# Kernel tuning notes

Hardware: AMD Instinct MI355X
Metric: run time of the kernel (lower is better)

Reference implementation:

```python
import jax, jax.numpy as jnp
import numpy as np

B, N, D = 512, 120, 64
NB = 8  # n_freq_bands
S_CLIP, DELTA_CLIP = 10.0, 5.0


def zc_rms(x, g, eps=1e-8):
    # zero-centred RMS norm
    x0 = x - x0_mean(x)
    return x0 * jax.lax.rsqrt(jnp.mean(x0 * x0, axis=-1, keepdims=True) + eps) * g


def x0_mean(x):
    return jnp.mean(x, axis=-1, keepdims=True)


def l2norm(x, eps=1e-8):
    return x * jax.lax.rsqrt(jnp.sum(x * x, axis=-1, keepdims=True) + eps)


def setup_inputs() -> dict:
    key = jax.random.key(0)
    ks = jax.random.split(key, 12)
    s = 1.0 / np.sqrt(D)
    return {
        "x": jax.random.normal(ks[0], (B, N, D), dtype=jnp.float32),
        "g_norm": jnp.ones((D,), jnp.float32),
        "Wq": jax.random.normal(ks[1], (D, D), jnp.float32) * s,
        "Wk": jax.random.normal(ks[2], (D, D), jnp.float32) * s,
        "Wv": jax.random.normal(ks[3], (D, D), jnp.float32) * s,
        "bv": jnp.zeros((D,), jnp.float32),
        "Wo": jax.random.normal(ks[4], (D, D), jnp.float32) * s,
        "bo": jnp.zeros((D,), jnp.float32),
        "g_post": jnp.ones((D,), jnp.float32),
        "W1": jax.random.normal(ks[5], (NB, 16), jnp.float32) * (1.0 / np.sqrt(NB)),
        "b1": jnp.zeros((16,), jnp.float32),
        "W2": jax.random.normal(ks[6], (16, 1), jnp.float32) * 0.25,
        "b2": jnp.full((1,), 0.5, jnp.float32),  # bias init 0.5 as in torch
    }


def _gamma(h, W1, b1, W2, b2):
    # FFT over embedding dim, band-averaged energies -> gate in [0.5, 0.99]
    fft = jnp.abs(jnp.fft.rfft(jax.lax.stop_gradient(h), axis=-1))  # (B,N,n_f)
    n_f = fft.shape[-1]
    bs = max(1, n_f // NB)
    bands = [fft[..., i * bs:min(i * bs + bs, n_f)].mean(-1) for i in range(NB)]
    energy = jnp.stack(bands, axis=-1)  # (B,N,NB)
    energy = energy / jnp.clip(jnp.sum(energy, axis=-1, keepdims=True), 1e-8)
    hdn = jax.nn.silu(energy @ W1 + b1)
    raw = jax.nn.sigmoid(hdn @ W2 + b2)  # (B,N,1)
    return 0.5 + 0.49 * raw


def reference(x, g_norm, Wq, Wk, Wv, bv, Wo, bo, g_post, W1, b1, W2, b2):
    h = zc_rms(x, g_norm)
    q = l2norm(h @ Wq)
    k = l2norm(h @ Wk)
    v = h @ Wv + bv
    gamma = _gamma(h, W1, b1, W2, b2)  # (B,N,1)

    # time-major for scan
    qT = jnp.moveaxis(q, 1, 0)      # (N,B,D)
    kT = jnp.moveaxis(k, 1, 0)
    vT = jnp.moveaxis(v, 1, 0)
    gT = jnp.moveaxis(gamma, 1, 0)  # (N,B,1)

    S0 = jnp.zeros((x.shape[0], D, D), x.dtype)

    def step(S, inp):
        q_t, k_t, v_t, g_t = inp
        pred = jnp.einsum('bde,be->bd', S, k_t)
        delta = jnp.clip(v_t - pred, -DELTA_CLIP, DELTA_CLIP)
        S = g_t[..., None] * S + delta[:, :, None] * k_t[:, None, :]
        S = jnp.clip(S, -S_CLIP, S_CLIP)
        o_t = jnp.einsum('bde,be->bd', S, q_t)
        return S, o_t

    _, outT = jax.lax.scan(step, S0, (qT, kT, vT, gT))
    out = jnp.moveaxis(outT, 0, 1)  # (B,N,D)
    out = zc_rms(out, g_post) @ Wo + bo  # dropout is identity at inference
    return x + out
```

## Files before the change

### kernel.cpp

```cpp
#include <hip/hip_runtime.h>
#include <math.h>

#define B_ 512
#define N_ 120

typedef __attribute__((ext_vector_type(8))) _Float16 f16x8;
typedef __attribute__((ext_vector_type(2))) _Float16 f16x2;
typedef __attribute__((ext_vector_type(4))) float f32x4;

#define OFF_WQ 0
#define OFF_WK 4096
#define OFF_WV 8192
#define OFF_T  12288
#define OFF_XF 16384
#define OFF_QS 0
#define OFF_KS 7680
#define OFF_VS 15360
#define OFF_OF 23040
#define OFF_WO 31232
#define LDS_F16 35328

__device__ __forceinline__ void mm4(f16x8 a0, f16x8 a1, const _Float16* wmat,
                                    int lane, f32x4* acc) {
    const f16x8* wv = (const f16x8*)wmat;
    #pragma unroll
    for (int nt = 0; nt < 4; ++nt) {
        f32x4 z = {0.f, 0.f, 0.f, 0.f};
        z = __builtin_amdgcn_mfma_f32_16x16x32_f16(a0, wv[nt * 128 + lane], z, 0, 0, 0);
        z = __builtin_amdgcn_mfma_f32_16x16x32_f16(a1, wv[nt * 128 + 64 + lane], z, 0, 0, 0);
        acc[nt] = z;
    }
}

__global__ __launch_bounds__(512, 4) void fused_kdn(
    const float* __restrict__ x, const float* __restrict__ g_norm,
    const float* __restrict__ Wq, const float* __restrict__ Wk,
    const float* __restrict__ Wv, const float* __restrict__ bv,
    const float* __restrict__ Wo, const float* __restrict__ bo,
    const float* __restrict__ g_post,
    const float* __restrict__ W1, const float* __restrict__ b1,
    const float* __restrict__ W2, const float* __restrict__ b2,
    float* out)
{
    __shared__ __align__(16) _Float16 L[LDS_F16];
    __shared__ float g_s[N_];
    __shared__ float bv_s[64], bo_s[64];
    __shared__ float sW1[128], sb1[16], sW2[16], sb2_s[1];

    int tid = threadIdx.x, wave = tid >> 6, lane = tid & 63;
    int b = blockIdx.x;

    if (tid < 128) sW1[tid] = W1[tid];
    if (tid >= 128 && tid < 144) sb1[tid - 128] = b1[tid - 128];
    if (tid >= 144 && tid < 160) sW2[tid - 144] = W2[tid - 144];
    if (tid == 160) sb2_s[0] = b2[0];
    if (tid >= 192 && tid < 256) bv_s[tid - 192] = bv[tid - 192];
    if (tid >= 256 && tid < 320) bo_s[tid - 256] = bo[tid - 256];
    if (tid < 128) {
        f16x8 z = {0, 0, 0, 0, 0, 0, 0, 0};
        *(f16x8*)&L[OFF_XF + 7168 + tid * 8] = z;
        *(f16x8*)&L[OFF_OF + 7168 + tid * 8] = z;
    }
    int sn = tid & 63, sk0 = (tid >> 6) * 8;
    int widx = (sn >> 4) * 1024 + (sk0 >> 5) * 512 + ((((sk0 >> 3) & 3) << 4) + (sn & 15)) * 8;
    {
        const float* Ws[4] = { Wq, Wk, Wv, Wo };
        const int woff[4] = { OFF_WQ, OFF_WK, OFF_WV, OFF_WO };
        #pragma unroll
        for (int m = 0; m < 4; ++m) {
            f16x8 pv;
            #pragma unroll
            for (int j = 0; j < 8; ++j) pv[j] = (_Float16)Ws[m][(sk0 + j) * 64 + sn];
            *(f16x8*)&L[woff[m] + widx] = pv;
        }
        f16x8 pv;
        int nn = sn & 31;
        #pragma unroll
        for (int j = 0; j < 8; ++j) {
            int kk = ((sk0 + j) * nn) & 63;
            float a = (float)kk * (6.283185307179586f / 64.0f);
            float s, c; __sincosf(a, &s, &c);
            pv[j] = (_Float16)((sn < 32) ? c : s);
        }
        *(f16x8*)&L[OFF_T + widx] = pv;
    }
    __syncthreads();

    const float* xb = x + (size_t)b * N_ * 64;
    float* ob_g = out + (size_t)b * N_ * 64;

    {
        float gn = g_norm[lane];
        int hbase = (lane >> 5) * 512 + ((lane >> 3) & 3) * 128 + (lane & 7);
        #pragma unroll 5
        for (int c = 0; c < 15; ++c) {
            int row = wave * 15 + c;
            float xv = xb[row * 64 + lane];
            float sx = xv, sxx = xv * xv;
            #pragma unroll
            for (int m = 1; m < 64; m <<= 1) { sx += __shfl_xor(sx, m); sxx += __shfl_xor(sxx, m); }
            float mean = sx * 0.015625f;
            float var  = sxx * 0.015625f - mean * mean;
            float h = (xv - mean) * rsqrtf(var + 1e-8f) * gn;
            float hp = __shfl_xor(h, 1);
            if (!(lane & 1)) {
                f16x2 pk2 = { (_Float16)h, (_Float16)hp };
                *(f16x2*)&L[OFF_XF + (row >> 4) * 1024 + (row & 15) * 8 + hbase] = pk2;
            }
        }
    }
    __syncthreads();

    int grp = lane >> 4, li = lane & 15;
    int rbase = wave * 16 + grp * 4;
    {
        const f16x8* hfv = (const f16x8*)(L + OFF_XF);
        f16x8 a0 = hfv[wave * 128 + lane];
        f16x8 a1 = hfv[wave * 128 + 64 + lane];
        f32x4 accT[4];

        mm4(a0, a1, L + OFF_T, lane, accT);
        {
            int gb2 = lane & 48;
            #pragma unroll
            for (int reg = 0; reg < 4; ++reg) {
                float re1 = accT[0][reg], re2 = accT[1][reg];
                float im1 = accT[2][reg], im2 = accT[3][reg];
                float m1 = sqrtf(fmaf(re1, re1, im1 * im1));
                float m2 = sqrtf(fmaf(re2, re2, im2 * im2));
                m1 += __shfl_xor(m1, 1); m2 += __shfl_xor(m2, 1);
                m1 += __shfl_xor(m1, 2); m2 += __shfl_xor(m2, 2);
                float e1 = m1 * 0.25f, e2 = m2 * 0.25f;
                float tot = e1 + e2;
                tot += __shfl_xor(tot, 4); tot += __shfl_xor(tot, 8);
                float rinv = 1.0f / fmaxf(tot, 1e-8f);
                float en1 = e1 * rinv, en2 = e2 * rinv;
                float hs = sb1[li];
                #pragma unroll
                for (int i = 0; i < 4; ++i)
                    hs = fmaf(__shfl(en1, gb2 + (i << 2)), sW1[i * 16 + li], hs);
                #pragma unroll
                for (int i = 0; i < 4; ++i)
                    hs = fmaf(__shfl(en2, gb2 + (i << 2)), sW1[(i + 4) * 16 + li], hs);
                float act = hs / (1.0f + __expf(-hs));
                float p = act * sW2[li];
                p += __shfl_xor(p, 1); p += __shfl_xor(p, 2);
                p += __shfl_xor(p, 4); p += __shfl_xor(p, 8);
                float raw = 1.0f / (1.0f + __expf(-(p + sb2_s[0])));
                int row = rbase + reg;
                if (li == 0 && row < N_) g_s[row] = fmaf(0.49f, raw, 0.5f);
            }
        }

        f32x4 accq[4], acck[4], accv[4];
        mm4(a0, a1, L + OFF_WQ, lane, accq);
        mm4(a0, a1, L + OFF_WK, lane, acck);
        mm4(a0, a1, L + OFF_WV, lane, accv);

        {
            f32x4 sq = accq[0]*accq[0] + accq[1]*accq[1] + accq[2]*accq[2] + accq[3]*accq[3];
            f32x4 sk = acck[0]*acck[0] + acck[1]*acck[1] + acck[2]*acck[2] + acck[3]*acck[3];
            #pragma unroll
            for (int reg = 0; reg < 4; ++reg) {
                float qs = sq[reg], ks = sk[reg];
                #pragma unroll
                for (int m = 1; m < 16; m <<= 1) { qs += __shfl_xor(qs, m); ks += __shfl_xor(ks, m); }
                float rq = rsqrtf(qs + 1e-8f), rk = rsqrtf(ks + 1e-8f);
                #pragma unroll
                for (int nt = 0; nt < 4; ++nt) { accq[nt][reg] *= rq; acck[nt][reg] *= rk; }
            }
            #pragma unroll
            for (int nt = 0; nt < 4; ++nt) {
                float bvn = bv_s[nt * 16 + li];
                #pragma unroll
                for (int reg = 0; reg < 4; ++reg) accv[nt][reg] += bvn;
            }
        }
        __syncthreads();

        #pragma unroll
        for (int reg = 0; reg < 4; ++reg) {
            int row = rbase + reg;
            if (row < N_) {
                int base = row * 64 + li;
                #pragma unroll
                for (int nt = 0; nt < 4; ++nt) {
                    L[OFF_QS + base + nt * 16] = (_Float16)accq[nt][reg];
                    L[OFF_KS + base + nt * 16] = (_Float16)acck[nt][reg];
                    L[OFF_VS + base + nt * 16] = (_Float16)accv[nt][reg];
                }
            }
        }
    }
    __syncthreads();

    {
        int g8 = lane & 7, dlo = lane >> 3;
        int d = wave * 8 + dlo;
        int co = g8 * 8;
        int dbase = (d >> 5) * 512 + ((d >> 3) & 3) * 128 + (d & 7);
        const _Float16* ks = L + OFF_KS;
        const _Float16* qs = L + OFF_QS;
        const _Float16* vs = L + OFF_VS;

        float S[8];
        #pragma unroll
        for (int j = 0; j < 8; ++j) S[j] = 0.f;

        f16x8 kh = *(const f16x8*)&ks[co];
        f16x8 qh = *(const f16x8*)&qs[co];
        _Float16 vh = vs[d];
        float gt = g_s[0];

        for (int t = 0; t < N_; ++t) {
            int tn = (t + 1 < N_) ? (t + 1) : t;
            f16x8 khn = *(const f16x8*)&ks[tn * 64 + co];
            f16x8 qhn = *(const f16x8*)&qs[tn * 64 + co];
            _Float16 vhn = vs[tn * 64 + d];
            float gtn = g_s[tn];

            float p0 = 0.f, p1 = 0.f, p2 = 0.f, p3 = 0.f;
            p0 = fmaf(S[0], (float)kh[0], p0); p1 = fmaf(S[1], (float)kh[1], p1);
            p2 = fmaf(S[2], (float)kh[2], p2); p3 = fmaf(S[3], (float)kh[3], p3);
            p0 = fmaf(S[4], (float)kh[4], p0); p1 = fmaf(S[5], (float)kh[5], p1);
            p2 = fmaf(S[6], (float)kh[6], p2); p3 = fmaf(S[7], (float)kh[7], p3);
            float p = (p0 + p1) + (p2 + p3);
            p += __shfl_xor(p, 1); p += __shfl_xor(p, 2); p += __shfl_xor(p, 4);

            float delta = __builtin_amdgcn_fmed3f((float)vh - p, -5.0f, 5.0f);

            float oa = 0.f, ob = 0.f;
#define UPD(j, oo) { float s = fmaf(delta, (float)kh[j], gt * S[j]);           \
                     s = __builtin_amdgcn_fmed3f(s, -10.f, 10.f); S[j] = s;    \
                     oo = fmaf(s, (float)qh[j], oo); }
            UPD(0, oa) UPD(1, ob) UPD(2, oa) UPD(3, ob)
            UPD(4, oa) UPD(5, ob) UPD(6, oa) UPD(7, ob)
#undef UPD
            float o = oa + ob;
            o += __shfl_xor(o, 1); o += __shfl_xor(o, 2); o += __shfl_xor(o, 4);
            if (g8 == 0)
                L[OFF_OF + (t >> 4) * 1024 + (t & 15) * 8 + dbase] = (_Float16)o;

            kh = khn; qh = qhn; vh = vhn; gt = gtn;
        }
    }
    __syncthreads();

    {
        float gp = g_post[lane];
        int hbase = (lane >> 5) * 512 + ((lane >> 3) & 3) * 128 + (lane & 7);
        #pragma unroll 5
        for (int c = 0; c < 15; ++c) {
            int row = wave * 15 + c;
            int ridx = OFF_OF + (row >> 4) * 1024 + (row & 15) * 8;
            float ov = (float)L[ridx + hbase];
            float sx = ov, sxx = ov * ov;
            #pragma unroll
            for (int m = 1; m < 64; m <<= 1) { sx += __shfl_xor(sx, m); sxx += __shfl_xor(sxx, m); }
            float mean = sx * 0.015625f;
            float var  = sxx * 0.015625f - mean * mean;
            float hn = (ov - mean) * rsqrtf(var + 1e-8f) * gp;
            float hp = __shfl_xor(hn, 1);
            if (!(lane & 1)) {
                f16x2 pk2 = { (_Float16)hn, (_Float16)hp };
                *(f16x2*)&L[ridx + hbase] = pk2;
            }
        }
    }
    __syncthreads();

    {
        const f16x8* hfv = (const f16x8*)(L + OFF_OF);
        f16x8 a0 = hfv[wave * 128 + lane];
        f16x8 a1 = hfv[wave * 128 + 64 + lane];
        f32x4 acc[4];
        mm4(a0, a1, L + OFF_WO, lane, acc);
        #pragma unroll
        for (int reg = 0; reg < 4; ++reg) {
            int row = rbase + reg;
            if (row < N_) {
                #pragma unroll
                for (int nt = 0; nt < 4; ++nt) {
                    int idx = row * 64 + nt * 16 + li;
                    ob_g[idx] = acc[nt][reg] + bo_s[nt * 16 + li] + xb[idx];
                }
            }
        }
    }
}

extern "C" void kernel_launch(void* const* d_in, const int* in_sizes, int n_in,
                              void* d_out, int out_size, void* d_ws, size_t ws_size,
                              hipStream_t stream)
{
    const float* x      = (const float*)d_in[0];
    const float* g_norm = (const float*)d_in[1];
    const float* Wq     = (const float*)d_in[2];
    const float* Wk     = (const float*)d_in[3];
    const float* Wv     = (const float*)d_in[4];
    const float* bv     = (const float*)d_in[5];
    const float* Wo     = (const float*)d_in[6];
    const float* bo     = (const float*)d_in[7];
    const float* g_post = (const float*)d_in[8];
    const float* W1     = (const float*)d_in[9];
    const float* b1     = (const float*)d_in[10];
    const float* W2     = (const float*)d_in[11];
    const float* b2     = (const float*)d_in[12];
    float* out = (float*)d_out;

    fused_kdn<<<B_, 512, 0, stream>>>(x, g_norm, Wq, Wk, Wv, bv, Wo, bo, g_post,
                                      W1, b1, W2, b2, out);
}
```

Measured before the change: 179.7 us.

## Fuse next-step prediction into state update and pack shuffle reductions in fp16

The recurrent scan now computes the next step's prediction S·k_{t+1} during the current state update, so each step needs one reduction instead of two serialized ones. The output and prediction partial sums are packed into a half2 and reduced together with a single set of xor-shuffles, halving cross-lane traffic. The gamma values are loaded four at a time as float4. This trades numerical precision, since the prediction and output reductions are now done in fp16, which could shift results relative to the fp32 reference.

```diff
diff --git a/kernel.cpp b/kernel.cpp
--- a/kernel.cpp
+++ b/kernel.cpp
@@ -7,6 +7,8 @@
 typedef __attribute__((ext_vector_type(8))) _Float16 f16x8;
 typedef __attribute__((ext_vector_type(2))) _Float16 f16x2;
 typedef __attribute__((ext_vector_type(4))) float f32x4;
+
+union PK { f16x2 h; int i; };
 
 #define OFF_WQ 0
 #define OFF_WK 4096
@@ -43,7 +45,7 @@
     float* out)
 {
     __shared__ __align__(16) _Float16 L[LDS_F16];
-    __shared__ float g_s[N_];
+    __shared__ __align__(16) float g_s[N_];
     __shared__ float bv_s[64], bo_s[64];
     __shared__ float sW1[128], sb1[16], sW2[16], sb2_s[1];
 
@@ -210,38 +212,44 @@
         f16x8 kh = *(const f16x8*)&ks[co];
         f16x8 qh = *(const f16x8*)&qs[co];
         _Float16 vh = vs[d];
-        float gt = g_s[0];
-
-        for (int t = 0; t < N_; ++t) {
-            int tn = (t + 1 < N_) ? (t + 1) : t;
-            f16x8 khn = *(const f16x8*)&ks[tn * 64 + co];
-            f16x8 qhn = *(const f16x8*)&qs[tn * 64 + co];
-            _Float16 vhn = vs[tn * 64 + d];
-            float gtn = g_s[tn];
-
-            float p0 = 0.f, p1 = 0.f, p2 = 0.f, p3 = 0.f;
-            p0 = fmaf(S[0], (float)kh[0], p0); p1 = fmaf(S[1], (float)kh[1], p1);
-            p2 = fmaf(S[2], (float)kh[2], p2); p3 = fmaf(S[3], (float)kh[3], p3);
-            p0 = fmaf(S[4], (float)kh[4], p0); p1 = fmaf(S[5], (float)kh[5], p1);
-            p2 = fmaf(S[6], (float)kh[6], p2); p3 = fmaf(S[7], (float)kh[7], p3);
-            float p = (p0 + p1) + (p2 + p3);
-            p += __shfl_xor(p, 1); p += __shfl_xor(p, 2); p += __shfl_xor(p, 4);
-
-            float delta = __builtin_amdgcn_fmed3f((float)vh - p, -5.0f, 5.0f);
-
-            float oa = 0.f, ob = 0.f;
-#define UPD(j, oo) { float s = fmaf(delta, (float)kh[j], gt * S[j]);           \
+        float pbc = 0.f;
+        float4 gq = *(const float4*)&g_s[0];
+
+        for (int t4 = 0; t4 < N_; t4 += 4) {
+            float4 gq_n = (t4 + 4 < N_) ? *(const float4*)&g_s[t4 + 4] : gq;
+            #pragma unroll
+            for (int j4 = 0; j4 < 4; ++j4) {
+                int t = t4 + j4;
+                int tn = (t + 1 < N_) ? (t + 1) : t;
+                f16x8 khn = *(const f16x8*)&ks[tn * 64 + co];
+                f16x8 qhn = *(const f16x8*)&qs[tn * 64 + co];
+                _Float16 vhn = vs[tn * 64 + d];
+                float gt = (j4 == 0) ? gq.x : (j4 == 1) ? gq.y : (j4 == 2) ? gq.z : gq.w;
+
+                float delta = __builtin_amdgcn_fmed3f((float)vh - pbc, -5.0f, 5.0f);
+
+                float oa = 0.f, ob = 0.f, pa = 0.f, pb = 0.f;
+#define UPD(j, oo, pp) { float s = fmaf(delta, (float)kh[j], gt * S[j]);       \
                      s = __builtin_amdgcn_fmed3f(s, -10.f, 10.f); S[j] = s;    \
-                     oo = fmaf(s, (float)qh[j], oo); }
-            UPD(0, oa) UPD(1, ob) UPD(2, oa) UPD(3, ob)
-            UPD(4, oa) UPD(5, ob) UPD(6, oa) UPD(7, ob)
+                     oo = fmaf(s, (float)qh[j], oo);                           \
+                     pp = fmaf(s, (float)khn[j], pp); }
+                UPD(0, oa, pa) UPD(1, ob, pb) UPD(2, oa, pa) UPD(3, ob, pb)
+                UPD(4, oa, pa) UPD(5, ob, pb) UPD(6, oa, pa) UPD(7, ob, pb)
 #undef UPD
-            float o = oa + ob;
-            o += __shfl_xor(o, 1); o += __shfl_xor(o, 2); o += __shfl_xor(o, 4);
-            if (g8 == 0)
-                L[OFF_OF + (t >> 4) * 1024 + (t & 15) * 8 + dbase] = (_Float16)o;
-
-            kh = khn; qh = qhn; vh = vhn; gt = gtn;
+                PK pk;
+                pk.h[0] = (_Float16)(oa + ob);
+                pk.h[1] = (_Float16)(pa + pb);
+                PK r1; r1.i = __shfl_xor(pk.i, 1); pk.h = pk.h + r1.h;
+                PK r2; r2.i = __shfl_xor(pk.i, 2); pk.h = pk.h + r2.h;
+                PK r4; r4.i = __shfl_xor(pk.i, 4); pk.h = pk.h + r4.h;
+
+                if (g8 == 0)
+                    L[OFF_OF + (t >> 4) * 1024 + (t & 15) * 8 + dbase] = pk.h[0];
+                pbc = (float)pk.h[1];
+
+                kh = khn; qh = qhn; vh = vhn;
+            }
+            gq = gq_n;
         }
     }
     __syncthreads();
```

After: 177.7 us. About the same (-1.1%).
